# Optimization experiments

Measured on AMD Instinct MI355X. Metric: run time of the kernel, lower is better.

Reference implementation:

```python
import jax, jax.numpy as jnp
import numpy as np

EMBED_DIM = 1024
NUM_HEADS = 16
HEAD_DIM = EMBED_DIM // NUM_HEADS
B, T = 4, 1024
NEG = -1.0e9
LN_EPS = 1e-5


def setup_inputs() -> dict:
    key = jax.random.key(0)
    ks = jax.random.split(key, 13)
    s = 1.0 / np.sqrt(EMBED_DIM)
    return {
        "query": jax.random.normal(ks[0], (B, T, EMBED_DIM), jnp.float32),
        "key": jax.random.normal(ks[1], (B, T, EMBED_DIM), jnp.float32),
        "value": jax.random.normal(ks[2], (B, T, EMBED_DIM), jnp.float32),
        "mask": jax.random.randint(ks[3], (B, 1, T, T), 0, 2, jnp.int32),
        "Wq": jax.random.normal(ks[4], (EMBED_DIM, EMBED_DIM), jnp.float32) * s,
        "bq": jnp.zeros((EMBED_DIM,), jnp.float32),
        "Wk": jax.random.normal(ks[5], (EMBED_DIM, EMBED_DIM), jnp.float32) * s,
        "bk": jnp.zeros((EMBED_DIM,), jnp.float32),
        "Wv": jax.random.normal(ks[6], (EMBED_DIM, EMBED_DIM), jnp.float32) * s,
        "bv": jnp.zeros((EMBED_DIM,), jnp.float32),
        "Wo": jax.random.normal(ks[7], (EMBED_DIM, EMBED_DIM), jnp.float32) * s,
        "bo": jnp.zeros((EMBED_DIM,), jnp.float32),
        "gamma": jnp.ones((EMBED_DIM,), jnp.float32),
        "beta": jnp.zeros((EMBED_DIM,), jnp.float32),
    }


def _split_heads(x):
    # (B, T, E) -> (B, H, T, D)
    b, t, _ = x.shape
    return x.reshape(b, t, NUM_HEADS, HEAD_DIM).transpose(0, 2, 1, 3)


def _mha(query, key, value, mask, Wq, bq, Wk, bk, Wv, bv, Wo, bo, gamma, beta,
         temperature=1.0):
    q = _split_heads(query @ Wq.T + bq)
    k = _split_heads(key @ Wk.T + bk)
    v = _split_heads(value @ Wv.T + bv)
    # scores: (B, H, T, T)
    scale = jnp.sqrt(jnp.float32(HEAD_DIM)) * temperature
    scores = jnp.einsum("bhqd,bhkd->bhqk", q, k) / scale
    scores = jnp.where(mask == 0, NEG, scores)
    scores = scores - jnp.max(scores, axis=-1, keepdims=True)
    # temperature >= 0.01 in this config, so the low-temperature hard-cutoff
    # branch is skipped (matches torch's Python-level `if temperature < 0.01`).
    scores = jnp.nan_to_num(scores, nan=0.0, posinf=1.0e9, neginf=-1.0e9)
    attn = jax.nn.softmax(scores, axis=-1)
    # eval mode: dropout is identity (self.training is False)
    out = jnp.einsum("bhqk,bhkd->bhqd", attn, v)  # (B, H, T, D)
    out = out.transpose(0, 2, 1, 3).reshape(query.shape[0], query.shape[1], EMBED_DIM)
    out = out @ Wo.T + bo
    # layer norm over embed_dim
    mu = jnp.mean(out, axis=-1, keepdims=True)
    var = jnp.mean(jnp.square(out - mu), axis=-1, keepdims=True)
    out = (out - mu) * jax.lax.rsqrt(var + LN_EPS) * gamma + beta
    return out


def reference(query, key, value, mask, Wq, bq, Wk, bk, Wv, bv, Wo, bo, gamma, beta):
    return _mha(query, key, value, mask, Wq, bq, Wk, bk, Wv, bv, Wo, bo, gamma, beta)
```

## Files before the change

kernel.cpp:

```cpp
#include <hip/hip_runtime.h>
#include <cmath>

#define T_SEQ 1024
#define EMB   1024
#define NH    16
#define HD    64
#define NB    4
#define BQ    64
#define BK    64

#define QSCALE 0.18033688011112042f
#define BIAS2  -1.44269504e9f

using frag8   = __attribute__((ext_vector_type(8))) short;
using f32x4   = __attribute__((ext_vector_type(4))) float;
using short4v = __attribute__((ext_vector_type(4))) short;
using short8v = __attribute__((ext_vector_type(8))) short;

__device__ inline short f2bf(float f) {
    union { float f; unsigned u; } x; x.f = f;
    unsigned r = (x.u + 0x7FFFu + ((x.u >> 16) & 1u)) >> 16;
    return (short)r;
}
__device__ inline float bf2f(unsigned short u) {
    union { unsigned u; float f; } x; x.u = ((unsigned)u) << 16;
    return x.f;
}
__device__ inline int cvt_pk_bf16(float lo, float hi) {
    int r;
    asm("v_cvt_pk_bf16_f32 %0, %1, %2" : "=v"(r) : "v"(lo), "v"(hi));
    return r;
}

__device__ inline void glds16(const short* g, short* l) {
    __builtin_amdgcn_global_load_lds(
        (const __attribute__((address_space(1))) void*)g,
        (__attribute__((address_space(3))) void*)l, 16, 0, 0);
}

struct ConvArgs { const float* src[7]; short* dst[7]; int n8[7]; };

__global__ __launch_bounds__(256) void convert_bf16(ConvArgs a) {
    const int y = blockIdx.y;
    const int t = blockIdx.x * 256 + threadIdx.x;
    if (t >= a.n8[y]) return;
    const float4* s = (const float4*)a.src[y];
    const float4 v0 = s[t * 2], v1 = s[t * 2 + 1];
    short8v o;
    o[0] = f2bf(v0.x); o[1] = f2bf(v0.y); o[2] = f2bf(v0.z); o[3] = f2bf(v0.w);
    o[4] = f2bf(v1.x); o[5] = f2bf(v1.y); o[6] = f2bf(v1.z); o[7] = f2bf(v1.w);
    *(short8v*)&a.dst[y][t * 8] = o;
}

__global__ __launch_bounds__(256) void convert_mask(
    const int* __restrict__ mask, short* __restrict__ dst)
{
    const int wave = threadIdx.x >> 6, lane = threadIdx.x & 63;
    const int tile = blockIdx.x * 4 + wave;
    const int bb   = tile >> 12;
    const int q16  = (tile >> 6) & 63;
    const int k16  = tile & 63;
    const int qrow = lane >> 2;
    const int col4 = (lane & 3) * 4;
    const int4 mv = *(const int4*)&mask[((size_t)bb * T_SEQ + q16 * 16 + qrow) * T_SEQ
                                        + k16 * 16 + col4];
    const short BB = f2bf(BIAS2);
    short4v o;
    o[0] = mv.x ? (short)0 : BB;
    o[1] = mv.y ? (short)0 : BB;
    o[2] = mv.z ? (short)0 : BB;
    o[3] = mv.w ? (short)0 : BB;
    *(short4v*)&dst[(size_t)tile * 256 + qrow * 16 + col4] = o;
}

struct GemmB { const short* A; const short* W; const float* bias; short* out; float scale; };
struct QkvArgs { GemmB g[3]; };

template <int MODE>
__device__ inline void gemm_core(const short* __restrict__ A,
                                 const short* __restrict__ W,
                                 const float* __restrict__ bias,
                                 float scale,
                                 short* __restrict__ outS,
                                 float* __restrict__ outF,
                                 int m0, int n0)
{
    __shared__ short As[2][128 * 32];
    __shared__ short Bs[2][128 * 32];

    const int tid  = threadIdx.x;
    const int wave = tid >> 6;
    const int lane = tid & 63;
    const int quad = lane >> 4;
    const int lm   = lane & 15;
    const int wr   = wave >> 1;
    const int wc   = wave & 1;
    const int K    = EMB;

    const int G0 = wave * 64 + lane, G1 = G0 + 256;
    const short* aSrc0 = A + (size_t)(m0 + (G0 >> 2)) * K + (G0 & 3) * 8;
    const short* aSrc1 = A + (size_t)(m0 + (G1 >> 2)) * K + (G1 & 3) * 8;
    const short* bSrc0 = W + (size_t)(n0 + (G0 >> 2)) * K + (G0 & 3) * 8;
    const short* bSrc1 = W + (size_t)(n0 + (G1 >> 2)) * K + (G1 & 3) * 8;
    short* aDst0 = &As[0][wave * 512];
    short* aDst1 = &As[0][2048 + wave * 512];
    short* bDst0 = &Bs[0][wave * 512];
    short* bDst1 = &Bs[0][2048 + wave * 512];

    f32x4 acc[4][4];
#pragma unroll
    for (int i = 0; i < 4; ++i)
#pragma unroll
        for (int j = 0; j < 4; ++j) acc[i][j] = (f32x4){0.f, 0.f, 0.f, 0.f};

    for (int kk = 0; kk < K; kk += 64) {
        __syncthreads();
        glds16(aSrc0 + kk,      aDst0);
        glds16(aSrc1 + kk,      aDst1);
        glds16(bSrc0 + kk,      bDst0);
        glds16(bSrc1 + kk,      bDst1);
        glds16(aSrc0 + kk + 32, aDst0 + 4096);
        glds16(aSrc1 + kk + 32, aDst1 + 4096);
        glds16(bSrc0 + kk + 32, bDst0 + 4096);
        glds16(bSrc1 + kk + 32, bDst1 + 4096);
        __syncthreads();

#pragma unroll
        for (int p = 0; p < 2; ++p) {
            frag8 aF[4], bF[4];
#pragma unroll
            for (int i = 0; i < 4; ++i)
                aF[i] = *(const frag8*)&As[p][(wr * 64 + i * 16 + lm) * 32 + quad * 8];
#pragma unroll
            for (int j = 0; j < 4; ++j)
                bF[j] = *(const frag8*)&Bs[p][(wc * 64 + j * 16 + lm) * 32 + quad * 8];
#pragma unroll
            for (int i = 0; i < 4; ++i)
#pragma unroll
                for (int j = 0; j < 4; ++j)
                    acc[i][j] = __builtin_amdgcn_mfma_f32_16x16x32_bf16(
                        aF[i], bF[j], acc[i][j], 0, 0, 0);
        }
    }

#pragma unroll
    for (int i = 0; i < 4; ++i)
#pragma unroll
        for (int j = 0; j < 4; ++j) {
            const int n = n0 + wc * 64 + j * 16 + lm;
            const float bv = bias[n];
#pragma unroll
            for (int rr = 0; rr < 4; ++rr) {
                const int m = m0 + wr * 64 + i * 16 + quad * 4 + rr;
                const float val = (acc[i][j][rr] + bv) * scale;
                if (MODE == 0) {
                    outF[((size_t)(m >> 4) * 64 + (n >> 4)) * 256 +
                         rr * 64 + quad * 16 + lm] = val;
                } else {
                    const int bb = m >> 10, tt = m & 1023;
                    const int h = n >> 6,  d  = n & 63;
                    const size_t bh = (size_t)bb * NH + h;
                    if (MODE == 1) {
                        outS[((bh * 64 + (tt >> 4)) * 8 + (d >> 3)) * 128 +
                             (tt & 15) * 8 + (d & 7)] = f2bf(val);
                    } else {
                        outS[((((bh * 16 + (tt >> 6)) * 2 + ((tt >> 5) & 1)) * 4 +
                              (d >> 4)) * 4 + ((tt >> 2) & 3)) * 128 +
                             (d & 15) * 8 + (((tt & 16) >> 2) | (tt & 3))] = f2bf(val);
                    }
                }
            }
        }
}

__global__ __launch_bounds__(256, 3) void gemm_qkv(QkvArgs args) {
    const int id = blockIdx.x + 8 * blockIdx.y + 256 * blockIdx.z;
    const int a  = id & 7;
    const int k2 = id >> 3;
    const int nb = k2 & 7;
    const int c  = k2 >> 3;
    const int pair = a * 12 + c;
    const int mb = pair & 31;
    const int zb = pair >> 5;
    const GemmB g = args.g[zb];
    if (zb < 2) gemm_core<1>(g.A, g.W, g.bias, g.scale, g.out, nullptr, mb * 128, nb * 128);
    else        gemm_core<2>(g.A, g.W, g.bias, g.scale, g.out, nullptr, mb * 128, nb * 128);
}

__global__ __launch_bounds__(256, 3) void gemm_wo(const short* __restrict__ A,
                                                  const short* __restrict__ W,
                                                  const float* __restrict__ bias,
                                                  float* __restrict__ out) {
    const int id = blockIdx.x + 8 * blockIdx.y;
    const int a  = id & 7;
    const int k2 = id >> 3;
    const int nb = k2 & 7;
    const int c  = k2 >> 3;
    const int mb = a * 4 + c;
    gemm_core<0>(A, W, bias, 1.0f, nullptr, out, mb * 128, nb * 128);
}

__global__ __launch_bounds__(512, 4) void flash_attn_mfma(
    const short* __restrict__ qf_, const short* __restrict__ kf_,
    const short* __restrict__ vf_, const short* __restrict__ mf_,
    short* __restrict__ out)
{
    __shared__ float Osh[4][17][64];

    const int tid  = threadIdx.x;
    const int wave = tid >> 6;
    const int lane = tid & 63;
    const int quad = lane >> 4;
    const int lm   = lane & 15;
    const int wq   = wave & 3;
    const int wk   = wave >> 2;

    const int id  = blockIdx.x;
    const int xcd = id & 7;
    const int idx = id >> 3;
    const int bh_i = xcd * 8 + (idx >> 4);
    const int b  = bh_i >> 4, h = bh_i & 15;
    const int q0 = (idx & 15) * BQ;
    const size_t bh = (size_t)bh_i;

    const short* qb_ = qf_ + (bh * 64 + (q0 >> 4) + wq) * 1024;
    const frag8 qfa = *(const frag8*)&qb_[(quad * 16 + lm) * 8];
    const frag8 qfb = *(const frag8*)&qb_[((quad + 4) * 16 + lm) * 8];

    const short* mrow = mf_ + ((size_t)b * 64 + (q0 >> 4) + wq) * (64 * 256)
                        + lm * 16 + quad * 4;

    f32x4 of[4];
#pragma unroll
    for (int dc = 0; dc < 4; ++dc) of[dc] = (f32x4){0.f, 0.f, 0.f, 0.f};
    float lsum = 0.f;

    for (int kt = 0; kt < 8; ++kt) {
        const int kt2 = wk * 8 + kt;

        frag8 vfr[2][4];
        const short* vbase = vf_ + (bh * 16 + kt2) * 4096;
#pragma unroll
        for (int hf = 0; hf < 2; ++hf)
#pragma unroll
            for (int dc = 0; dc < 4; ++dc)
                vfr[hf][dc] = *(const frag8*)
                    &vbase[((hf * 4 + dc) * 4 + quad) * 128 + lm * 8];

        short4v mb[4];
#pragma unroll
        for (int kc = 0; kc < 4; ++kc)
            mb[kc] = *(const short4v*)&mrow[(kt2 * 4 + kc) * 256];

        f32x4 s[4];
#pragma unroll
        for (int kc = 0; kc < 4; ++kc) {
            const short* kbase = kf_ + (bh * 64 + kt2 * 4 + kc) * 1024;
            const frag8 kfa = *(const frag8*)&kbase[(quad * 16 + lm) * 8];
            const frag8 kfb = *(const frag8*)&kbase[((quad + 4) * 16 + lm) * 8];
            f32x4 a = (f32x4){ bf2f((unsigned short)mb[kc][0]),
                               bf2f((unsigned short)mb[kc][1]),
                               bf2f((unsigned short)mb[kc][2]),
                               bf2f((unsigned short)mb[kc][3]) };
            a = __builtin_amdgcn_mfma_f32_16x16x32_bf16(kfa, qfa, a, 0, 0, 0);
            a = __builtin_amdgcn_mfma_f32_16x16x32_bf16(kfb, qfb, a, 0, 0, 0);
            s[kc] = a;
        }

#pragma unroll
        for (int kc = 0; kc < 4; ++kc) {
            s[kc][0] = exp2f(s[kc][0]); s[kc][1] = exp2f(s[kc][1]);
            s[kc][2] = exp2f(s[kc][2]); s[kc][3] = exp2f(s[kc][3]);
            lsum += (s[kc][0] + s[kc][1]) + (s[kc][2] + s[kc][3]);
        }

        union { int i[4]; frag8 f; } ua, ub;
        ua.i[0] = cvt_pk_bf16(s[0][0], s[0][1]);
        ua.i[1] = cvt_pk_bf16(s[0][2], s[0][3]);
        ua.i[2] = cvt_pk_bf16(s[1][0], s[1][1]);
        ua.i[3] = cvt_pk_bf16(s[1][2], s[1][3]);
        ub.i[0] = cvt_pk_bf16(s[2][0], s[2][1]);
        ub.i[1] = cvt_pk_bf16(s[2][2], s[2][3]);
        ub.i[2] = cvt_pk_bf16(s[3][0], s[3][1]);
        ub.i[3] = cvt_pk_bf16(s[3][2], s[3][3]);

        __builtin_amdgcn_s_setprio(1);
#pragma unroll
        for (int dc = 0; dc < 4; ++dc) {
            of[dc] = __builtin_amdgcn_mfma_f32_16x16x32_bf16(vfr[0][dc], ua.f, of[dc], 0, 0, 0);
            of[dc] = __builtin_amdgcn_mfma_f32_16x16x32_bf16(vfr[1][dc], ub.f, of[dc], 0, 0, 0);
        }
        __builtin_amdgcn_s_setprio(0);
    }

    if (wk) {
#pragma unroll
        for (int c = 0; c < 16; ++c) Osh[wq][c][lane] = of[c >> 2][c & 3];
        Osh[wq][16][lane] = lsum;
    }
    __syncthreads();
    if (!wk) {
#pragma unroll
        for (int c = 0; c < 16; ++c) of[c >> 2][c & 3] += Osh[wq][c][lane];
        lsum += Osh[wq][16][lane];

        lsum += __shfl_xor(lsum, 16);
        lsum += __shfl_xor(lsum, 32);
        const float inv = 1.0f / lsum;

        short* ob = out + ((size_t)b * T_SEQ + q0 + wq * 16 + lm) * EMB + h * HD;
#pragma unroll
        for (int dc = 0; dc < 4; ++dc) {
            short4v o4;
#pragma unroll
            for (int rr = 0; rr < 4; ++rr) o4[rr] = f2bf(of[dc][rr] * inv);
            *(short4v*)&ob[dc * 16 + quad * 4] = o4;
        }
    }
}

__global__ __launch_bounds__(256) void layernorm_k(
    const float* __restrict__ x, const float* __restrict__ gamma,
    const float* __restrict__ beta, float* __restrict__ out)
{
    __shared__ float ws1[4], ws2[4];
    const int tid = threadIdx.x;
    const int row = blockIdx.x;
    const int m16 = row >> 4, rr = row & 3, qd = (row >> 2) & 3;

    const float4 v = *(const float4*)&x[((size_t)m16 * 64 + (tid >> 2)) * 256 +
                                        rr * 64 + qd * 16 + (tid & 3) * 4];
    float s  = v.x + v.y + v.z + v.w;
    float ss = v.x * v.x + v.y * v.y + v.z * v.z + v.w * v.w;
#pragma unroll
    for (int off = 32; off > 0; off >>= 1) {
        s  += __shfl_down(s, off);
        ss += __shfl_down(ss, off);
    }
    if ((tid & 63) == 0) { ws1[tid >> 6] = s; ws2[tid >> 6] = ss; }
    __syncthreads();
    if (tid == 0) {
        const float a = ws1[0] + ws1[1] + ws1[2] + ws1[3];
        const float bsum = ws2[0] + ws2[1] + ws2[2] + ws2[3];
        const float mu = a * (1.0f / EMB);
        const float var = bsum * (1.0f / EMB) - mu * mu;
        ws1[0] = mu;
        ws2[0] = rsqrtf(var + 1e-5f);
    }
    __syncthreads();
    const float mu = ws1[0], rstd = ws2[0];

    const float4 g = *(const float4*)&gamma[tid * 4];
    const float4 bt = *(const float4*)&beta[tid * 4];
    float4 r;
    r.x = (v.x - mu) * rstd * g.x + bt.x;
    r.y = (v.y - mu) * rstd * g.y + bt.y;
    r.z = (v.z - mu) * rstd * g.z + bt.z;
    r.w = (v.w - mu) * rstd * g.w + bt.w;
    *(float4*)&out[(size_t)row * EMB + tid * 4] = r;
}

extern "C" void kernel_launch(void* const* d_in, const int* in_sizes, int n_in,
                              void* d_out, int out_size, void* d_ws, size_t ws_size,
                              hipStream_t stream) {
    const float* query = (const float*)d_in[0];
    const float* key_i = (const float*)d_in[1];
    const float* value = (const float*)d_in[2];
    const int*   mask  = (const int*)d_in[3];
    const float* Wq = (const float*)d_in[4];
    const float* bq = (const float*)d_in[5];
    const float* Wk = (const float*)d_in[6];
    const float* bk = (const float*)d_in[7];
    const float* Wv = (const float*)d_in[8];
    const float* bv = (const float*)d_in[9];
    const float* Wo = (const float*)d_in[10];
    const float* bo = (const float*)d_in[11];
    const float* gamma = (const float*)d_in[12];
    const float* beta  = (const float*)d_in[13];

    const size_t SZ = (size_t)NB * T_SEQ * EMB;
    const size_t WZ = (size_t)EMB * EMB;
    short* sws = (short*)d_ws;
    short* q_bf  = sws;
    short* k_bf  = sws + SZ;
    short* v_bf  = sws + 2 * SZ;
    short* w_bf  = sws + 3 * SZ;
    short* qh    = sws + 4 * SZ;
    short* kh    = sws + 5 * SZ;
    short* vh    = sws + 6 * SZ;
    short* maskb = sws + 7 * SZ;
    short* attnb = q_bf;
    float* projb = (float*)(sws + SZ);

    ConvArgs ca;
    ca.src[0] = query; ca.dst[0] = q_bf;          ca.n8[0] = (int)(SZ / 8);
    ca.src[1] = key_i; ca.dst[1] = k_bf;          ca.n8[1] = (int)(SZ / 8);
    ca.src[2] = value; ca.dst[2] = v_bf;          ca.n8[2] = (int)(SZ / 8);
    ca.src[3] = Wq;    ca.dst[3] = w_bf;          ca.n8[3] = (int)(WZ / 8);
    ca.src[4] = Wk;    ca.dst[4] = w_bf + WZ;     ca.n8[4] = (int)(WZ / 8);
    ca.src[5] = Wv;    ca.dst[5] = w_bf + 2 * WZ; ca.n8[5] = (int)(WZ / 8);
    ca.src[6] = Wo;    ca.dst[6] = w_bf + 3 * WZ; ca.n8[6] = (int)(WZ / 8);
    convert_bf16<<<dim3((SZ / 8 + 255) / 256, 7), 256, 0, stream>>>(ca);

    convert_mask<<<dim3(NB * 64 * 64 / 4), 256, 0, stream>>>(mask, maskb);

    QkvArgs qa;
    qa.g[0] = { q_bf, w_bf,          bq, qh, QSCALE };
    qa.g[1] = { k_bf, w_bf + WZ,     bk, kh, 1.0f };
    qa.g[2] = { v_bf, w_bf + 2 * WZ, bv, vh, 1.0f };
    gemm_qkv<<<dim3(EMB / 128, NB * T_SEQ / 128, 3), 256, 0, stream>>>(qa);

    flash_attn_mfma<<<dim3(T_SEQ / BQ * NH * NB), 512, 0, stream>>>(qh, kh, vh, maskb, attnb);

    gemm_wo<<<dim3(EMB / 128, NB * T_SEQ / 128), 256, 0, stream>>>(
        attnb, w_bf + 3 * WZ, bo, projb);

    layernorm_k<<<dim3(NB * T_SEQ), 256, 0, stream>>>(projb, gamma, beta, (float*)d_out);
}
```

Baseline: 255.7 us.

## Stage K/V tiles in LDS via global-to-LDS loads and compute row sums with MFMA

K and V tiles for each key step are now loaded cooperatively into shared memory with direct global-to-LDS copies, so the four query waves of a block share one fetch instead of each reading K/V from global memory. Softmax row sums move from scalar adds plus cross-lane shuffles to two extra MFMAs against a ones vector. This adds two block barriers per key iteration and reuses the LDS buffer for the final reduction, with an extra barrier before that reuse.

```diff
diff --git a/kernel.cpp b/kernel.cpp
--- a/kernel.cpp
+++ b/kernel.cpp
@@ -205,7 +205,7 @@
     const short* __restrict__ vf_, const short* __restrict__ mf_,
     short* __restrict__ out)
 {
-    __shared__ float Osh[4][17][64];
+    __shared__ short KV[4][4096];
 
     const int tid  = threadIdx.x;
     const int wave = tid >> 6;
@@ -223,6 +223,12 @@
     const int q0 = (idx & 15) * BQ;
     const size_t bh = (size_t)bh_i;
 
+    const int  sbuf  = wave >> 1;
+    const int  shalf = (wave & 1) * 2048;
+    const short* sb = ((sbuf < 2) ? kf_ : vf_) + bh * 65536
+                      + (size_t)(sbuf & 1) * 32768 + shalf + lane * 8;
+    short* dstb = &KV[sbuf][shalf];
+
     const short* qb_ = qf_ + (bh * 64 + (q0 >> 4) + wq) * 1024;
     const frag8 qfa = *(const frag8*)&qb_[(quad * 16 + lm) * 8];
     const frag8 qfb = *(const frag8*)&qb_[((quad + 4) * 16 + lm) * 8];
@@ -230,34 +236,34 @@
     const short* mrow = mf_ + ((size_t)b * 64 + (q0 >> 4) + wq) * (64 * 256)
                         + lm * 16 + quad * 4;
 
+    union { int i[4]; frag8 f; } ones;
+    ones.i[0] = ones.i[1] = ones.i[2] = ones.i[3] = 0x3F803F80;
+
     f32x4 of[4];
 #pragma unroll
     for (int dc = 0; dc < 4; ++dc) of[dc] = (f32x4){0.f, 0.f, 0.f, 0.f};
-    float lsum = 0.f;
+    f32x4 ls = (f32x4){0.f, 0.f, 0.f, 0.f};
 
     for (int kt = 0; kt < 8; ++kt) {
         const int kt2 = wk * 8 + kt;
 
-        frag8 vfr[2][4];
-        const short* vbase = vf_ + (bh * 16 + kt2) * 4096;
-#pragma unroll
-        for (int hf = 0; hf < 2; ++hf)
-#pragma unroll
-            for (int dc = 0; dc < 4; ++dc)
-                vfr[hf][dc] = *(const frag8*)
-                    &vbase[((hf * 4 + dc) * 4 + quad) * 128 + lm * 8];
+        __syncthreads();
+#pragma unroll
+        for (int it = 0; it < 4; ++it)
+            glds16(sb + kt * 4096 + it * 512, dstb + it * 512);
 
         short4v mb[4];
 #pragma unroll
         for (int kc = 0; kc < 4; ++kc)
             mb[kc] = *(const short4v*)&mrow[(kt2 * 4 + kc) * 256];
+        __syncthreads();
 
         f32x4 s[4];
 #pragma unroll
         for (int kc = 0; kc < 4; ++kc) {
-            const short* kbase = kf_ + (bh * 64 + kt2 * 4 + kc) * 1024;
-            const frag8 kfa = *(const frag8*)&kbase[(quad * 16 + lm) * 8];
-            const frag8 kfb = *(const frag8*)&kbase[((quad + 4) * 16 + lm) * 8];
+            const short* kb = &KV[wk][kc * 1024];
+            const frag8 kfa = *(const frag8*)&kb[(quad * 16 + lm) * 8];
+            const frag8 kfb = *(const frag8*)&kb[((quad + 4) * 16 + lm) * 8];
             f32x4 a = (f32x4){ bf2f((unsigned short)mb[kc][0]),
                                bf2f((unsigned short)mb[kc][1]),
                                bf2f((unsigned short)mb[kc][2]),
@@ -271,7 +277,6 @@
         for (int kc = 0; kc < 4; ++kc) {
             s[kc][0] = exp2f(s[kc][0]); s[kc][1] = exp2f(s[kc][1]);
             s[kc][2] = exp2f(s[kc][2]); s[kc][3] = exp2f(s[kc][3]);
-            lsum += (s[kc][0] + s[kc][1]) + (s[kc][2] + s[kc][3]);
         }
 
         union { int i[4]; frag8 f; } ua, ub;
@@ -287,25 +292,28 @@
         __builtin_amdgcn_s_setprio(1);
 #pragma unroll
         for (int dc = 0; dc < 4; ++dc) {
-            of[dc] = __builtin_amdgcn_mfma_f32_16x16x32_bf16(vfr[0][dc], ua.f, of[dc], 0, 0, 0);
-            of[dc] = __builtin_amdgcn_mfma_f32_16x16x32_bf16(vfr[1][dc], ub.f, of[dc], 0, 0, 0);
-        }
+            const frag8 v0 = *(const frag8*)&KV[2 + wk][(dc * 4 + quad) * 128 + lm * 8];
+            const frag8 v1 = *(const frag8*)&KV[2 + wk][((4 + dc) * 4 + quad) * 128 + lm * 8];
+            of[dc] = __builtin_amdgcn_mfma_f32_16x16x32_bf16(v0, ua.f, of[dc], 0, 0, 0);
+            of[dc] = __builtin_amdgcn_mfma_f32_16x16x32_bf16(v1, ub.f, of[dc], 0, 0, 0);
+        }
+        ls = __builtin_amdgcn_mfma_f32_16x16x32_bf16(ones.f, ua.f, ls, 0, 0, 0);
+        ls = __builtin_amdgcn_mfma_f32_16x16x32_bf16(ones.f, ub.f, ls, 0, 0, 0);
         __builtin_amdgcn_s_setprio(0);
     }
 
+    float* Osh = (float*)&KV[0][0];
+    __syncthreads();
     if (wk) {
 #pragma unroll
-        for (int c = 0; c < 16; ++c) Osh[wq][c][lane] = of[c >> 2][c & 3];
-        Osh[wq][16][lane] = lsum;
+        for (int c = 0; c < 16; ++c) Osh[(wq * 17 + c) * 64 + lane] = of[c >> 2][c & 3];
+        Osh[(wq * 17 + 16) * 64 + lane] = ls[0];
     }
     __syncthreads();
     if (!wk) {
 #pragma unroll
-        for (int c = 0; c < 16; ++c) of[c >> 2][c & 3] += Osh[wq][c][lane];
-        lsum += Osh[wq][16][lane];
-
-        lsum += __shfl_xor(lsum, 16);
-        lsum += __shfl_xor(lsum, 32);
+        for (int c = 0; c < 16; ++c) of[c >> 2][c & 3] += Osh[(wq * 17 + c) * 64 + lane];
+        const float lsum = ls[0] + Osh[(wq * 17 + 16) * 64 + lane];
         const float inv = 1.0f / lsum;
 
         short* ob = out + ((size_t)b * T_SEQ + q0 + wq * 16 + lm) * EMB + h * HD;
```

Measured after the change: 247.7 us. 3.1% less time.
